# Kernel tuning notes

Hardware: AMD Instinct MI355X
Metric: run time of the kernel (lower is better)

The kernel has to match this reference:

```python
import jax, jax.numpy as jnp
import numpy as np

B, C, L = 8, 256, 4096
OC = C // 2  # out_channels default
EPS = 1e-5


def setup_inputs() -> dict:
    key = jax.random.key(0)
    ks = jax.random.split(key, 12)
    s_in = 1.0 / np.sqrt(C)   # conv1d default init scale (kaiming-uniform-ish)
    s_oc = 1.0 / np.sqrt(OC)
    return {
        "x": jax.random.normal(ks[0], (B, C, L), dtype=jnp.float32),
        "g_w": jax.random.uniform(ks[1], (OC, C), jnp.float32, -s_in, s_in),
        "g_b": jax.random.uniform(ks[2], (OC,), jnp.float32, -s_in, s_in),
        # theta/phi weights: nn.init.normal_(w, 0.02) -> mean 0.02, std 1
        "theta_w": 0.02 + jax.random.normal(ks[3], (OC, C), dtype=jnp.float32),
        "theta_b": jax.random.uniform(ks[4], (OC,), jnp.float32, -s_in, s_in),
        "phi_w": 0.02 + jax.random.normal(ks[5], (OC, C), dtype=jnp.float32),
        "phi_b": jax.random.uniform(ks[6], (OC,), jnp.float32, -s_in, s_in),
        "W_w": jax.random.uniform(ks[7], (C, OC), jnp.float32, -s_oc, s_oc),
        "W_b": jax.random.uniform(ks[8], (C,), jnp.float32, -s_oc, s_oc),
        # BN affine: init to zero in the original; use small random for a meaningful test
        "gamma": 0.1 * jax.random.normal(ks[9], (C,), dtype=jnp.float32),
        "beta": 0.1 * jax.random.normal(ks[10], (C,), dtype=jnp.float32),
    }


def reference(x, g_w, g_b, theta_w, theta_b, phi_w, phi_b, W_w, W_b, gamma, beta):
    # x: (b, c, l). 1x1 conv == per-position linear map over channels.
    g_x = jnp.einsum('oc,bcl->bol', g_w, x) + g_b[None, :, None]        # (b, oc, l)
    theta_x = jnp.einsum('oc,bcl->bol', theta_w, x) + theta_b[None, :, None]
    phi_x = jnp.einsum('oc,bcl->bol', phi_w, x) + phi_b[None, :, None]
    # f = theta^T phi : (b, l, l) quadratic score matrix (no softmax)
    f = jnp.einsum('bok,bom->bkm', theta_x, phi_x)
    N = f.shape[-1]
    # y = (f @ g^T) / N, returned in (b, oc, l) layout
    y = jnp.einsum('bkm,bom->bok', f, g_x) / N
    W_y = jnp.einsum('co,bol->bcl', W_w, y) + W_b[None, :, None]        # (b, c, l)
    # BatchNorm1d (training mode: batch statistics over (b, l), biased var)
    mean = jnp.mean(W_y, axis=(0, 2), keepdims=True)
    var = jnp.mean((W_y - mean) ** 2, axis=(0, 2), keepdims=True)
    W_y = (W_y - mean) * jax.lax.rsqrt(var + EPS)
    W_y = gamma[None, :, None] * W_y + beta[None, :, None]
    return W_y + x  # residual
```

## Files before the change

### kernel.cpp

```cpp
#include <hip/hip_runtime.h>
#include <hip/hip_bf16.h>

#define B_ 8
#define C_ 256
#define OC_ 128
#define L_ 4096
#define EPS_ 1e-5f
#define SPLITK 8

typedef unsigned short u16;
typedef __attribute__((ext_vector_type(4))) unsigned short u16x4;
typedef __attribute__((ext_vector_type(8))) unsigned short u16x8;
typedef __attribute__((ext_vector_type(4))) float f32x4;
typedef __attribute__((ext_vector_type(8))) short bf16x8;

__device__ inline u16 f2bf(float f) {
  union { __hip_bfloat16 h; u16 u; } v;
  v.h = __float2bfloat16(f);
  return v.u;
}
__device__ inline float bf2f(u16 u) {
  union { float f; unsigned u; } v;
  v.u = ((unsigned)u) << 16;
  return v.f;
}

__device__ inline void gload_lds16(const void* g, void* lds) {
  __builtin_amdgcn_global_load_lds(
      (const __attribute__((address_space(1))) unsigned int*)g,
      (__attribute__((address_space(3))) unsigned int*)lds, 16, 0, 0);
}

__device__ inline float blockReduceSum(float v, float* red, int nthreads) {
  int tid = threadIdx.x;
  red[tid] = v;
  __syncthreads();
  for (int s = nthreads >> 1; s > 0; s >>= 1) {
    if (tid < s) red[tid] += red[tid + s];
    __syncthreads();
  }
  float r = red[0];
  __syncthreads();
  return r;
}

__global__ __launch_bounds__(256) void k_cvt(const float* __restrict__ x,
                                             u16* __restrict__ Xb,
                                             u16* __restrict__ XbT) {
  __shared__ u16 T[64][72];
  const int b = blockIdx.z, c0 = blockIdx.y * 64, l0 = blockIdx.x * 64;
  const int tid = threadIdx.x;
#pragma unroll
  for (int it = 0; it < 4; ++it) {
    int idx = it * 256 + tid;
    int row = idx >> 4;
    int col = (idx & 15) << 2;
    size_t gi = ((size_t)(b * C_ + c0 + row)) * L_ + l0 + col;
    float4 v = *(const float4*)(x + gi);
    u16 u0 = f2bf(v.x), u1 = f2bf(v.y), u2 = f2bf(v.z), u3 = f2bf(v.w);
    u16x4 u = {u0, u1, u2, u3};
    *(u16x4*)(Xb + gi) = u;
    T[row][col] = u0; T[row][col + 1] = u1; T[row][col + 2] = u2; T[row][col + 3] = u3;
  }
  __syncthreads();
#pragma unroll
  for (int it = 0; it < 4; ++it) {
    int idx = it * 256 + tid;
    int lrow = idx >> 4;
    int ccol = (idx & 15) << 2;
    u16x4 u = {T[ccol][lrow], T[ccol + 1][lrow], T[ccol + 2][lrow], T[ccol + 3][lrow]};
    *(u16x4*)(XbT + ((size_t)b * L_ + l0 + lrow) * C_ + c0 + ccol) = u;
  }
}

__global__ __launch_bounds__(256) void k_rowsum(const u16* __restrict__ Xb,
                                                float* __restrict__ s) {
  int row = blockIdx.x;
  const u16x8* xr = (const u16x8*)(Xb + (size_t)row * L_);
  float acc = 0.f;
  for (int i = threadIdx.x; i < L_ / 8; i += 256) {
    u16x8 v = xr[i];
#pragma unroll
    for (int j = 0; j < 8; j++) acc += bf2f(v[j]);
  }
  __shared__ float red[256];
  float tot = blockReduceSum(acc, red, 256);
  if (threadIdx.x == 0) s[row] = tot;
}

__global__ __launch_bounds__(256) void k_xxt(const u16* __restrict__ Xb,
                                             float* __restrict__ Spart) {
  const int b = blockIdx.z, split = blockIdx.y;
  const int ti = blockIdx.x >> 1, tj = blockIdx.x & 1;
  __shared__ u16 lds[2 * 128 * 64];
  const int tid = threadIdx.x, lane = tid & 63;
  const int wid = tid >> 6, wr = wid >> 1, wc = wid & 1;
  const u16* Arows = Xb + ((size_t)b * C_ + ti * 128) * L_;
  const u16* Brows = Xb + ((size_t)b * C_ + tj * 128) * L_;
  const int k0 = split * (L_ / SPLITK);
  f32x4 acc[4][4] = {};
  for (int kt = 0; kt < L_ / SPLITK; kt += 64) {
    __syncthreads();
#pragma unroll
    for (int ch = 0; ch < 4; ch++) {
      int d = ch * 4096 + tid * 16;
      int row = d >> 7;
      int kb = (d & 127) ^ ((row & 7) << 4);
      gload_lds16(Arows + (size_t)row * L_ + k0 + kt + (kb >> 1), (char*)lds + d);
      gload_lds16(Brows + (size_t)row * L_ + k0 + kt + (kb >> 1), (char*)lds + 16384 + d);
    }
    asm volatile("s_waitcnt vmcnt(0)" ::: "memory");
    __syncthreads();
#pragma unroll
    for (int ks = 0; ks < 2; ks++) {
      bf16x8 af[4], bfr[4];
#pragma unroll
      for (int m = 0; m < 4; m++) {
        int row = wr * 64 + m * 16 + (lane & 15);
        int kb = ((ks << 6) + ((lane >> 4) << 4)) ^ ((row & 7) << 4);
        af[m] = *(const bf16x8*)((const char*)lds + row * 128 + kb);
      }
#pragma unroll
      for (int n = 0; n < 4; n++) {
        int row = wc * 64 + n * 16 + (lane & 15);
        int kb = ((ks << 6) + ((lane >> 4) << 4)) ^ ((row & 7) << 4);
        bfr[n] = *(const bf16x8*)((const char*)lds + 16384 + row * 128 + kb);
      }
#pragma unroll
      for (int m = 0; m < 4; m++)
#pragma unroll
        for (int n = 0; n < 4; n++)
          acc[m][n] = __builtin_amdgcn_mfma_f32_16x16x32_bf16(af[m], bfr[n], acc[m][n], 0, 0, 0);
    }
  }
  float* Sp = Spart + ((size_t)split * B_ + b) * C_ * C_;
#pragma unroll
  for (int m = 0; m < 4; m++)
#pragma unroll
    for (int n = 0; n < 4; n++) {
      int r0 = ti * 128 + wr * 64 + m * 16 + ((lane >> 4) << 2);
      int c0 = tj * 128 + wc * 64 + n * 16 + (lane & 15);
#pragma unroll
      for (int r = 0; r < 4; r++)
        Sp[(size_t)(r0 + r) * C_ + c0] = acc[m][n][r];
    }
}

__global__ __launch_bounds__(256) void k_sreduce(const float* __restrict__ Spart,
                                                 float* __restrict__ S) {
  size_t idx = (size_t)blockIdx.x * 256 + threadIdx.x;
  float acc = 0.f;
  for (int sp = 0; sp < SPLITK; sp++) acc += Spart[(size_t)sp * B_ * C_ * C_ + idx];
  S[idx] = acc;
}

__global__ __launch_bounds__(256) void k_mid1(const float* __restrict__ S,
                                              const float* __restrict__ s,
                                              const float* __restrict__ phi_w,
                                              const float* __restrict__ phi_b,
                                              const float* __restrict__ g_w,
                                              const float* __restrict__ g_b,
                                              float* __restrict__ M) {
  const int b = blockIdx.x >> 7, op = blockIdx.x & 127;
  const int tid = threadIdx.x;
  __shared__ float sl[C_], pw[C_], t2[C_], red[256];
  sl[tid] = s[b * C_ + tid];
  pw[tid] = phi_w[op * C_ + tid];
  __syncthreads();
  float ps_op = blockReduceSum(pw[tid] * sl[tid], red, 256);
  float phb = phi_b[op];
  const float* Sb = S + (size_t)b * C_ * C_;
  float t1 = 0.f;
  for (int cp = 0; cp < C_; cp++) t1 += pw[cp] * Sb[(size_t)cp * C_ + tid];
  t2[tid] = t1 + phb * sl[tid];
  __syncthreads();
  if (tid < OC_) {
    int o = tid;
    const float* gr = g_w + o * C_;
    float acc = 0.f;
    for (int c = 0; c < C_; c++) acc += t2[c] * gr[c];
    M[((size_t)b * OC_ + op) * OC_ + o] = acc + (ps_op + (float)L_ * phb) * g_b[o];
  }
}

__global__ __launch_bounds__(128) void k_mid2(const float* __restrict__ M,
                                              const float* __restrict__ W_w,
                                              const float* __restrict__ theta_w,
                                              const float* __restrict__ theta_b,
                                              const float* __restrict__ W_b,
                                              float* __restrict__ Q,
                                              float* __restrict__ q) {
  const int b = blockIdx.x >> 8, c = blockIdx.x & 255;
  const int tid = threadIdx.x;
  __shared__ float wr_[OC_], U_s[OC_], red[OC_];
  wr_[tid] = W_w[c * OC_ + tid];
  __syncthreads();
  const float* Mb = M + (size_t)b * OC_ * OC_;
  float acc = 0.f;
  for (int o = 0; o < OC_; o++) acc += wr_[o] * Mb[(size_t)tid * OC_ + o];
  acc *= (1.0f / (float)L_);
  U_s[tid] = acc;
  float tot = blockReduceSum(acc * theta_b[tid], red, OC_);
  if (tid == 0) q[b * C_ + c] = tot + W_b[c];
#pragma unroll
  for (int h = 0; h < 2; h++) {
    int ch = tid + h * OC_;
    float a2 = 0.f;
    for (int op = 0; op < OC_; op++) a2 += U_s[op] * theta_w[(size_t)op * C_ + ch];
    Q[((size_t)b * C_ + c) * C_ + ch] = a2;
  }
}

__global__ __launch_bounds__(256) void k_stats(const float* __restrict__ Q,
                                               const float* __restrict__ S,
                                               const float* __restrict__ s,
                                               const float* __restrict__ q,
                                               float* __restrict__ sum1,
                                               float* __restrict__ sum2) {
  int b = blockIdx.x >> 8, c = blockIdx.x & 255;
  __shared__ float qrow[C_];
  qrow[threadIdx.x] = Q[((size_t)b * C_ + c) * C_ + threadIdx.x];
  __syncthreads();
  const float* Sb = S + (size_t)b * C_ * C_;
  float r = 0.f;
  for (int cp = 0; cp < C_; cp++) r += qrow[cp] * Sb[(size_t)cp * C_ + threadIdx.x];
  __shared__ float red[C_];
  float e2 = blockReduceSum(r * qrow[threadIdx.x], red, C_);
  float qs = blockReduceSum(qrow[threadIdx.x] * s[b * C_ + threadIdx.x], red, C_);
  if (threadIdx.x == 0) {
    float qv = q[b * C_ + c];
    sum1[b * C_ + c] = qs + (float)L_ * qv;
    sum2[b * C_ + c] = e2 + 2.f * qv * qs + (float)L_ * qv * qv;
  }
}

__global__ __launch_bounds__(256) void k_build(const float* __restrict__ Q,
                                               const float* __restrict__ q,
                                               const float* __restrict__ sum1,
                                               const float* __restrict__ sum2,
                                               const float* __restrict__ gamma,
                                               const float* __restrict__ beta,
                                               u16* __restrict__ Qsb,
                                               float* __restrict__ qp) {
  int b = blockIdx.x >> 8, c = blockIdx.x & 255;
  float m = 0.f, e = 0.f;
  for (int bb = 0; bb < B_; bb++) {
    m += sum1[bb * C_ + c];
    e += sum2[bb * C_ + c];
  }
  const float inv_n = 1.f / (float)(B_ * L_);
  m *= inv_n;
  e *= inv_n;
  float var = e - m * m;
  float gsc = gamma[c] * rsqrtf(var + EPS_);
  size_t base = ((size_t)b * C_ + c) * C_;
  Qsb[base + threadIdx.x] = f2bf(gsc * Q[base + threadIdx.x]);
  if (threadIdx.x == 0) qp[b * C_ + c] = gsc * (q[b * C_ + c] - m) + beta[c];
}

__global__ __launch_bounds__(256) void k_out(const u16* __restrict__ Qsb,
                                             const float* __restrict__ qp,
                                             const u16* __restrict__ XbT,
                                             const u16* __restrict__ Xb,
                                             float* __restrict__ out) {
  const int b = blockIdx.z, ct = blockIdx.y, lt = blockIdx.x;
  __shared__ u16 lds[2 * 128 * 64];
  const int tid = threadIdx.x, lane = tid & 63;
  const int wid = tid >> 6, wr = wid >> 1, wc = wid & 1;
  const u16* Abase = Qsb + ((size_t)b * C_ + ct * 128) * C_;
  const u16* Bbase = XbT + ((size_t)b * L_ + lt * 128) * C_;
  f32x4 acc[4][4] = {};
  for (int k0 = 0; k0 < C_; k0 += 64) {
    __syncthreads();
#pragma unroll
    for (int ch = 0; ch < 4; ch++) {
      int d = ch * 4096 + tid * 16;
      int row = d >> 7;
      int kb = (d & 127) ^ ((row & 7) << 4);
      gload_lds16(Abase + (size_t)row * C_ + k0 + (kb >> 1), (char*)lds + d);
      gload_lds16(Bbase + (size_t)row * C_ + k0 + (kb >> 1), (char*)lds + 16384 + d);
    }
    asm volatile("s_waitcnt vmcnt(0)" ::: "memory");
    __syncthreads();
#pragma unroll
    for (int ks = 0; ks < 2; ks++) {
      bf16x8 af[4], bfr[4];
#pragma unroll
      for (int m = 0; m < 4; m++) {
        int row = wr * 64 + m * 16 + (lane & 15);
        int kb = ((ks << 6) + ((lane >> 4) << 4)) ^ ((row & 7) << 4);
        af[m] = *(const bf16x8*)((const char*)lds + row * 128 + kb);
      }
#pragma unroll
      for (int n = 0; n < 4; n++) {
        int row = wc * 64 + n * 16 + (lane & 15);
        int kb = ((ks << 6) + ((lane >> 4) << 4)) ^ ((row & 7) << 4);
        bfr[n] = *(const bf16x8*)((const char*)lds + 16384 + row * 128 + kb);
      }
#pragma unroll
      for (int m = 0; m < 4; m++)
#pragma unroll
        for (int n = 0; n < 4; n++)
          acc[m][n] = __builtin_amdgcn_mfma_f32_16x16x32_bf16(af[m], bfr[n], acc[m][n], 0, 0, 0);
    }
  }
#pragma unroll
  for (int m = 0; m < 4; m++)
#pragma unroll
    for (int n = 0; n < 4; n++) {
      int c = ct * 128 + wr * 64 + m * 16 + ((lane >> 4) << 2);
      int l = lt * 128 + wc * 64 + n * 16 + (lane & 15);
#pragma unroll
      for (int r = 0; r < 4; r++) {
        size_t gi = ((size_t)b * C_ + c + r) * L_ + l;
        out[gi] = acc[m][n][r] + bf2f(Xb[gi]) + qp[b * C_ + c + r];
      }
    }
}

extern "C" void kernel_launch(void* const* d_in, const int* in_sizes, int n_in,
                              void* d_out, int out_size, void* d_ws, size_t ws_size,
                              hipStream_t stream) {
  const float* x       = (const float*)d_in[0];
  const float* g_w     = (const float*)d_in[1];
  const float* g_b     = (const float*)d_in[2];
  const float* theta_w = (const float*)d_in[3];
  const float* theta_b = (const float*)d_in[4];
  const float* phi_w   = (const float*)d_in[5];
  const float* phi_b   = (const float*)d_in[6];
  const float* W_w     = (const float*)d_in[7];
  const float* W_b     = (const float*)d_in[8];
  const float* gamma   = (const float*)d_in[9];
  const float* beta    = (const float*)d_in[10];
  float* out = (float*)d_out;

  float* ws = (float*)d_ws;
  size_t off = 0;
  float* Spart = ws + off; off += (size_t)SPLITK * B_ * C_ * C_;
  float* S     = ws + off; off += (size_t)B_ * C_ * C_;
  float* s_    = ws + off; off += B_ * C_;
  float* M     = ws + off; off += (size_t)B_ * OC_ * OC_;
  float* qv    = ws + off; off += B_ * C_;
  float* Q     = ws + off; off += (size_t)B_ * C_ * C_;
  float* sum1  = ws + off; off += B_ * C_;
  float* sum2  = ws + off; off += B_ * C_;
  float* qp    = ws + off; off += B_ * C_;
  u16* Qsb = (u16*)(ws + off); off += (size_t)B_ * C_ * C_ / 2;
  u16* Xb  = (u16*)(ws + off); off += (size_t)B_ * C_ * L_ / 2;
  u16* XbT = (u16*)(ws + off); off += (size_t)B_ * C_ * L_ / 2;

  k_cvt<<<dim3(L_ / 64, C_ / 64, B_), 256, 0, stream>>>(x, Xb, XbT);
  k_rowsum<<<B_ * C_, 256, 0, stream>>>(Xb, s_);
  k_xxt<<<dim3(4, SPLITK, B_), 256, 0, stream>>>(Xb, Spart);
  k_sreduce<<<(B_ * C_ * C_) / 256, 256, 0, stream>>>(Spart, S);
  k_mid1<<<B_ * OC_, 256, 0, stream>>>(S, s_, phi_w, phi_b, g_w, g_b, M);
  k_mid2<<<B_ * C_, 128, 0, stream>>>(M, W_w, theta_w, theta_b, W_b, Q, qv);
  k_stats<<<B_ * C_, 256, 0, stream>>>(Q, S, s_, qv, sum1, sum2);
  k_build<<<B_ * C_, 256, 0, stream>>>(Q, qv, sum1, sum2, gamma, beta, Qsb, qp);
  k_out<<<dim3(L_ / 128, C_ / 128, B_), 256, 0, stream>>>(Qsb, qp, XbT, Xb, out);
}
```

Measured before the change: 143.1 us.

## Fuse rowsum, stats and build kernels into neighbours; cut launch count

The row sums of x are computed as per-tile partials inside the conversion kernel and finished in the split-K reduce kernel, which also transposes g_w. The stats and build kernels are folded into mid2 and the output GEMM: BN scale and shift are computed per tile, and Q is scaled and converted to bf16 on the fly from global memory rather than staged in LDS. mid1 and mid2 use transposed layouts for coalesced reads. This removes three launches and the Qsb round trip, but every output tile now re-reads fp32 Q from global and converts it per MFMA fragment, and the row sums now come from fp32 values instead of bf16.

```diff
diff --git a/kernel.cpp b/kernel.cpp
--- a/kernel.cpp
+++ b/kernel.cpp
@@ -10,7 +10,6 @@
 
 typedef unsigned short u16;
 typedef __attribute__((ext_vector_type(4))) unsigned short u16x4;
-typedef __attribute__((ext_vector_type(8))) unsigned short u16x8;
 typedef __attribute__((ext_vector_type(4))) float f32x4;
 typedef __attribute__((ext_vector_type(8))) short bf16x8;
 
@@ -46,8 +45,10 @@
 
 __global__ __launch_bounds__(256) void k_cvt(const float* __restrict__ x,
                                              u16* __restrict__ Xb,
-                                             u16* __restrict__ XbT) {
-  __shared__ u16 T[64][72];
+                                             u16* __restrict__ XbT,
+                                             float* __restrict__ spartial) {
+  __shared__ u16 T[64][73];
+  __shared__ float P[64][17];
   const int b = blockIdx.z, c0 = blockIdx.y * 64, l0 = blockIdx.x * 64;
   const int tid = threadIdx.x;
 #pragma unroll
@@ -61,8 +62,15 @@
     u16x4 u = {u0, u1, u2, u3};
     *(u16x4*)(Xb + gi) = u;
     T[row][col] = u0; T[row][col + 1] = u1; T[row][col + 2] = u2; T[row][col + 3] = u3;
-  }
-  __syncthreads();
+    P[row][idx & 15] = v.x + v.y + v.z + v.w;
+  }
+  __syncthreads();
+  if (tid < 64) {
+    float acc = 0.f;
+#pragma unroll
+    for (int j = 0; j < 16; j++) acc += P[tid][j];
+    spartial[(size_t)(b * C_ + c0 + tid) * 64 + blockIdx.x] = acc;
+  }
 #pragma unroll
   for (int it = 0; it < 4; ++it) {
     int idx = it * 256 + tid;
@@ -71,21 +79,6 @@
     u16x4 u = {T[ccol][lrow], T[ccol + 1][lrow], T[ccol + 2][lrow], T[ccol + 3][lrow]};
     *(u16x4*)(XbT + ((size_t)b * L_ + l0 + lrow) * C_ + c0 + ccol) = u;
   }
-}
-
-__global__ __launch_bounds__(256) void k_rowsum(const u16* __restrict__ Xb,
-                                                float* __restrict__ s) {
-  int row = blockIdx.x;
-  const u16x8* xr = (const u16x8*)(Xb + (size_t)row * L_);
-  float acc = 0.f;
-  for (int i = threadIdx.x; i < L_ / 8; i += 256) {
-    u16x8 v = xr[i];
-#pragma unroll
-    for (int j = 0; j < 8; j++) acc += bf2f(v[j]);
-  }
-  __shared__ float red[256];
-  float tot = blockReduceSum(acc, red, 256);
-  if (threadIdx.x == 0) s[row] = tot;
 }
 
 __global__ __launch_bounds__(256) void k_xxt(const u16* __restrict__ Xb,
@@ -147,20 +140,43 @@
 }
 
 __global__ __launch_bounds__(256) void k_sreduce(const float* __restrict__ Spart,
-                                                 float* __restrict__ S) {
-  size_t idx = (size_t)blockIdx.x * 256 + threadIdx.x;
-  float acc = 0.f;
-  for (int sp = 0; sp < SPLITK; sp++) acc += Spart[(size_t)sp * B_ * C_ * C_ + idx];
-  S[idx] = acc;
+                                                 const float* __restrict__ spartial,
+                                                 const float* __restrict__ g_w,
+                                                 float* __restrict__ S,
+                                                 float* __restrict__ s,
+                                                 float* __restrict__ gwT) {
+  const int bid = blockIdx.x, tid = threadIdx.x;
+  if (bid < (B_ * C_ * C_) / 256) {
+    size_t idx = (size_t)bid * 256 + tid;
+    float acc = 0.f;
+    for (int sp = 0; sp < SPLITK; sp++) acc += Spart[(size_t)sp * B_ * C_ * C_ + idx];
+    S[idx] = acc;
+  } else if (bid < (B_ * C_ * C_) / 256 + (B_ * C_) / 256) {
+    int idx2 = (bid - (B_ * C_ * C_) / 256) * 256 + tid;
+    const float4* sp = (const float4*)(spartial + (size_t)idx2 * 64);
+    float acc = 0.f;
+#pragma unroll
+    for (int i = 0; i < 16; i++) { float4 v = sp[i]; acc += v.x + v.y + v.z + v.w; }
+    s[idx2] = acc;
+  } else {
+    int t = bid - ((B_ * C_ * C_) / 256 + (B_ * C_) / 256);
+    int o = t * 8 + (tid & 7);
+    int cbase = (tid >> 3) * 8;
+#pragma unroll
+    for (int k = 0; k < 8; k++) {
+      int c = cbase + k;
+      gwT[c * OC_ + o] = g_w[o * C_ + c];
+    }
+  }
 }
 
 __global__ __launch_bounds__(256) void k_mid1(const float* __restrict__ S,
                                               const float* __restrict__ s,
                                               const float* __restrict__ phi_w,
                                               const float* __restrict__ phi_b,
-                                              const float* __restrict__ g_w,
+                                              const float* __restrict__ gwT,
                                               const float* __restrict__ g_b,
-                                              float* __restrict__ M) {
+                                              float* __restrict__ MT) {
   const int b = blockIdx.x >> 7, op = blockIdx.x & 127;
   const int tid = threadIdx.x;
   __shared__ float sl[C_], pw[C_], t2[C_], red[256];
@@ -174,101 +190,105 @@
   for (int cp = 0; cp < C_; cp++) t1 += pw[cp] * Sb[(size_t)cp * C_ + tid];
   t2[tid] = t1 + phb * sl[tid];
   __syncthreads();
+  const int o = tid & 127, half = tid >> 7;
+  float part = 0.f;
+  for (int cc = 0; cc < 128; cc++) {
+    int cidx = half * 128 + cc;
+    part += t2[cidx] * gwT[cidx * OC_ + o];
+  }
+  red[tid] = part;
+  __syncthreads();
   if (tid < OC_) {
-    int o = tid;
-    const float* gr = g_w + o * C_;
-    float acc = 0.f;
-    for (int c = 0; c < C_; c++) acc += t2[c] * gr[c];
-    M[((size_t)b * OC_ + op) * OC_ + o] = acc + (ps_op + (float)L_ * phb) * g_b[o];
-  }
-}
-
-__global__ __launch_bounds__(128) void k_mid2(const float* __restrict__ M,
-                                              const float* __restrict__ W_w,
-                                              const float* __restrict__ theta_w,
-                                              const float* __restrict__ theta_b,
-                                              const float* __restrict__ W_b,
-                                              float* __restrict__ Q,
-                                              float* __restrict__ q) {
+    float val = red[tid] + red[tid + 128] + (ps_op + (float)L_ * phb) * g_b[tid];
+    MT[((size_t)b * OC_ + tid) * OC_ + op] = val;
+  }
+}
+
+__global__ __launch_bounds__(128) void k_mid2stats(const float* __restrict__ MT,
+                                                   const float* __restrict__ W_w,
+                                                   const float* __restrict__ theta_w,
+                                                   const float* __restrict__ theta_b,
+                                                   const float* __restrict__ W_b,
+                                                   const float* __restrict__ S,
+                                                   const float* __restrict__ s,
+                                                   float* __restrict__ Q,
+                                                   float* __restrict__ qv,
+                                                   float* __restrict__ sum1,
+                                                   float* __restrict__ sum2) {
   const int b = blockIdx.x >> 8, c = blockIdx.x & 255;
   const int tid = threadIdx.x;
-  __shared__ float wr_[OC_], U_s[OC_], red[OC_];
+  __shared__ float wr_[OC_], U_s[OC_], red[OC_], qrow[C_];
   wr_[tid] = W_w[c * OC_ + tid];
   __syncthreads();
-  const float* Mb = M + (size_t)b * OC_ * OC_;
+  const float* MTb = MT + (size_t)b * OC_ * OC_;
   float acc = 0.f;
-  for (int o = 0; o < OC_; o++) acc += wr_[o] * Mb[(size_t)tid * OC_ + o];
+  for (int o = 0; o < OC_; o++) acc += wr_[o] * MTb[(size_t)o * OC_ + tid];
   acc *= (1.0f / (float)L_);
   U_s[tid] = acc;
   float tot = blockReduceSum(acc * theta_b[tid], red, OC_);
-  if (tid == 0) q[b * C_ + c] = tot + W_b[c];
+  float q_val = tot + W_b[c];
+  if (tid == 0) qv[b * C_ + c] = q_val;
+  float a2[2];
 #pragma unroll
   for (int h = 0; h < 2; h++) {
     int ch = tid + h * OC_;
-    float a2 = 0.f;
-    for (int op = 0; op < OC_; op++) a2 += U_s[op] * theta_w[(size_t)op * C_ + ch];
-    Q[((size_t)b * C_ + c) * C_ + ch] = a2;
-  }
-}
-
-__global__ __launch_bounds__(256) void k_stats(const float* __restrict__ Q,
-                                               const float* __restrict__ S,
-                                               const float* __restrict__ s,
-                                               const float* __restrict__ q,
-                                               float* __restrict__ sum1,
-                                               float* __restrict__ sum2) {
-  int b = blockIdx.x >> 8, c = blockIdx.x & 255;
-  __shared__ float qrow[C_];
-  qrow[threadIdx.x] = Q[((size_t)b * C_ + c) * C_ + threadIdx.x];
+    float a = 0.f;
+    for (int op = 0; op < OC_; op++) a += U_s[op] * theta_w[(size_t)op * C_ + ch];
+    a2[h] = a;
+    qrow[ch] = a;
+    Q[((size_t)b * C_ + c) * C_ + ch] = a;
+  }
   __syncthreads();
   const float* Sb = S + (size_t)b * C_ * C_;
-  float r = 0.f;
-  for (int cp = 0; cp < C_; cp++) r += qrow[cp] * Sb[(size_t)cp * C_ + threadIdx.x];
-  __shared__ float red[C_];
-  float e2 = blockReduceSum(r * qrow[threadIdx.x], red, C_);
-  float qs = blockReduceSum(qrow[threadIdx.x] * s[b * C_ + threadIdx.x], red, C_);
-  if (threadIdx.x == 0) {
-    float qv = q[b * C_ + c];
-    sum1[b * C_ + c] = qs + (float)L_ * qv;
-    sum2[b * C_ + c] = e2 + 2.f * qv * qs + (float)L_ * qv * qv;
-  }
-}
-
-__global__ __launch_bounds__(256) void k_build(const float* __restrict__ Q,
-                                               const float* __restrict__ q,
-                                               const float* __restrict__ sum1,
-                                               const float* __restrict__ sum2,
-                                               const float* __restrict__ gamma,
-                                               const float* __restrict__ beta,
-                                               u16* __restrict__ Qsb,
-                                               float* __restrict__ qp) {
-  int b = blockIdx.x >> 8, c = blockIdx.x & 255;
-  float m = 0.f, e = 0.f;
-  for (int bb = 0; bb < B_; bb++) {
-    m += sum1[bb * C_ + c];
-    e += sum2[bb * C_ + c];
-  }
-  const float inv_n = 1.f / (float)(B_ * L_);
-  m *= inv_n;
-  e *= inv_n;
-  float var = e - m * m;
-  float gsc = gamma[c] * rsqrtf(var + EPS_);
-  size_t base = ((size_t)b * C_ + c) * C_;
-  Qsb[base + threadIdx.x] = f2bf(gsc * Q[base + threadIdx.x]);
-  if (threadIdx.x == 0) qp[b * C_ + c] = gsc * (q[b * C_ + c] - m) + beta[c];
-}
-
-__global__ __launch_bounds__(256) void k_out(const u16* __restrict__ Qsb,
-                                             const float* __restrict__ qp,
+  float rq = 0.f, qssum = 0.f;
+#pragma unroll
+  for (int h = 0; h < 2; h++) {
+    int ch = tid + h * OC_;
+    float r = 0.f;
+    for (int cp = 0; cp < C_; cp++) r += qrow[cp] * Sb[(size_t)cp * C_ + ch];
+    rq += r * a2[h];
+    qssum += a2[h] * s[b * C_ + ch];
+  }
+  float e2 = blockReduceSum(rq, red, OC_);
+  float qs = blockReduceSum(qssum, red, OC_);
+  if (tid == 0) {
+    sum1[b * C_ + c] = qs + (float)L_ * q_val;
+    sum2[b * C_ + c] = e2 + 2.f * q_val * qs + (float)L_ * q_val * q_val;
+  }
+}
+
+__global__ __launch_bounds__(256) void k_out(const float* __restrict__ Q,
+                                             const float* __restrict__ qv,
+                                             const float* __restrict__ sum1,
+                                             const float* __restrict__ sum2,
+                                             const float* __restrict__ gamma,
+                                             const float* __restrict__ beta,
                                              const u16* __restrict__ XbT,
                                              const u16* __restrict__ Xb,
                                              float* __restrict__ out) {
   const int b = blockIdx.z, ct = blockIdx.y, lt = blockIdx.x;
-  __shared__ u16 lds[2 * 128 * 64];
+  __shared__ u16 lds[128 * 64];
+  __shared__ float gsc_s[128], qp_s[128];
   const int tid = threadIdx.x, lane = tid & 63;
   const int wid = tid >> 6, wr = wid >> 1, wc = wid & 1;
-  const u16* Abase = Qsb + ((size_t)b * C_ + ct * 128) * C_;
+  if (tid < 128) {
+    int c = ct * 128 + tid;
+    float m = 0.f, e = 0.f;
+#pragma unroll
+    for (int bb = 0; bb < B_; bb++) {
+      m += sum1[bb * C_ + c];
+      e += sum2[bb * C_ + c];
+    }
+    const float inv_n = 1.f / (float)(B_ * L_);
+    m *= inv_n;
+    e *= inv_n;
+    float var = e - m * m;
+    float g = gamma[c] * rsqrtf(var + EPS_);
+    gsc_s[tid] = g;
+    qp_s[tid] = g * (qv[b * C_ + c] - m) + beta[c];
+  }
   const u16* Bbase = XbT + ((size_t)b * L_ + lt * 128) * C_;
+  const float* Abase = Q + ((size_t)b * C_ + ct * 128) * C_;
   f32x4 acc[4][4] = {};
   for (int k0 = 0; k0 < C_; k0 += 64) {
     __syncthreads();
@@ -277,8 +297,7 @@
       int d = ch * 4096 + tid * 16;
       int row = d >> 7;
       int kb = (d & 127) ^ ((row & 7) << 4);
-      gload_lds16(Abase + (size_t)row * C_ + k0 + (kb >> 1), (char*)lds + d);
-      gload_lds16(Bbase + (size_t)row * C_ + k0 + (kb >> 1), (char*)lds + 16384 + d);
+      gload_lds16(Bbase + (size_t)row * C_ + k0 + (kb >> 1), (char*)lds + d);
     }
     asm volatile("s_waitcnt vmcnt(0)" ::: "memory");
     __syncthreads();
@@ -288,14 +307,23 @@
 #pragma unroll
       for (int m = 0; m < 4; m++) {
         int row = wr * 64 + m * 16 + (lane & 15);
-        int kb = ((ks << 6) + ((lane >> 4) << 4)) ^ ((row & 7) << 4);
-        af[m] = *(const bf16x8*)((const char*)lds + row * 128 + kb);
+        int kk = k0 + ks * 32 + ((lane >> 4) << 3);
+        float g = gsc_s[row];
+        const float* src = Abase + (size_t)row * C_ + kk;
+        float4 v0 = *(const float4*)src;
+        float4 v1 = *(const float4*)(src + 4);
+        bf16x8 a;
+        a[0] = (short)f2bf(g * v0.x); a[1] = (short)f2bf(g * v0.y);
+        a[2] = (short)f2bf(g * v0.z); a[3] = (short)f2bf(g * v0.w);
+        a[4] = (short)f2bf(g * v1.x); a[5] = (short)f2bf(g * v1.y);
+        a[6] = (short)f2bf(g * v1.z); a[7] = (short)f2bf(g * v1.w);
+        af[m] = a;
       }
 #pragma unroll
       for (int n = 0; n < 4; n++) {
         int row = wc * 64 + n * 16 + (lane & 15);
         int kb = ((ks << 6) + ((lane >> 4) << 4)) ^ ((row & 7) << 4);
-        bfr[n] = *(const bf16x8*)((const char*)lds + 16384 + row * 128 + kb);
+        bfr[n] = *(const bf16x8*)((const char*)lds + row * 128 + kb);
       }
 #pragma unroll
       for (int m = 0; m < 4; m++)
@@ -308,12 +336,13 @@
   for (int m = 0; m < 4; m++)
 #pragma unroll
     for (int n = 0; n < 4; n++) {
-      int c = ct * 128 + wr * 64 + m * 16 + ((lane >> 4) << 2);
+      int cl = wr * 64 + m * 16 + ((lane >> 4) << 2);
+      int c = ct * 128 + cl;
       int l = lt * 128 + wc * 64 + n * 16 + (lane & 15);
 #pragma unroll
       for (int r = 0; r < 4; r++) {
         size_t gi = ((size_t)b * C_ + c + r) * L_ + l;
-        out[gi] = acc[m][n][r] + bf2f(Xb[gi]) + qp[b * C_ + c + r];
+        out[gi] = acc[m][n][r] + bf2f(Xb[gi]) + qp_s[cl + r];
       }
     }
 }
@@ -336,26 +365,26 @@
 
   float* ws = (float*)d_ws;
   size_t off = 0;
-  float* Spart = ws + off; off += (size_t)SPLITK * B_ * C_ * C_;
-  float* S     = ws + off; off += (size_t)B_ * C_ * C_;
-  float* s_    = ws + off; off += B_ * C_;
-  float* M     = ws + off; off += (size_t)B_ * OC_ * OC_;
-  float* qv    = ws + off; off += B_ * C_;
-  float* Q     = ws + off; off += (size_t)B_ * C_ * C_;
-  float* sum1  = ws + off; off += B_ * C_;
-  float* sum2  = ws + off; off += B_ * C_;
-  float* qp    = ws + off; off += B_ * C_;
-  u16* Qsb = (u16*)(ws + off); off += (size_t)B_ * C_ * C_ / 2;
+  float* Spart    = ws + off; off += (size_t)SPLITK * B_ * C_ * C_;
+  float* S        = ws + off; off += (size_t)B_ * C_ * C_;
+  float* spartial = ws + off; off += (size_t)B_ * C_ * 64;
+  float* s_       = ws + off; off += B_ * C_;
+  float* gwT      = ws + off; off += C_ * OC_;
+  float* MT       = ws + off; off += (size_t)B_ * OC_ * OC_;
+  float* qv       = ws + off; off += B_ * C_;
+  float* Q        = ws + off; off += (size_t)B_ * C_ * C_;
+  float* sum1     = ws + off; off += B_ * C_;
+  float* sum2     = ws + off; off += B_ * C_;
   u16* Xb  = (u16*)(ws + off); off += (size_t)B_ * C_ * L_ / 2;
   u16* XbT = (u16*)(ws + off); off += (size_t)B_ * C_ * L_ / 2;
 
-  k_cvt<<<dim3(L_ / 64, C_ / 64, B_), 256, 0, stream>>>(x, Xb, XbT);
-  k_rowsum<<<B_ * C_, 256, 0, stream>>>(Xb, s_);
+  k_cvt<<<dim3(L_ / 64, C_ / 64, B_), 256, 0, stream>>>(x, Xb, XbT, spartial);
   k_xxt<<<dim3(4, SPLITK, B_), 256, 0, stream>>>(Xb, Spart);
-  k_sreduce<<<(B_ * C_ * C_) / 256, 256, 0, stream>>>(Spart, S);
-  k_mid1<<<B_ * OC_, 256, 0, stream>>>(S, s_, phi_w, phi_b, g_w, g_b, M);
-  k_mid2<<<B_ * C_, 128, 0, stream>>>(M, W_w, theta_w, theta_b, W_b, Q, qv);
-  k_stats<<<B_ * C_, 256, 0, stream>>>(Q, S, s_, qv, sum1, sum2);
-  k_build<<<B_ * C_, 256, 0, stream>>>(Q, qv, sum1, sum2, gamma, beta, Qsb, qp);
-  k_out<<<dim3(L_ / 128, C_ / 128, B_), 256, 0, stream>>>(Qsb, qp, XbT, Xb, out);
-}
+  k_sreduce<<<(B_ * C_ * C_) / 256 + (B_ * C_) / 256 + 16, 256, 0, stream>>>(
+      Spart, spartial, g_w, S, s_, gwT);
+  k_mid1<<<B_ * OC_, 256, 0, stream>>>(S, s_, phi_w, phi_b, gwT, g_b, MT);
+  k_mid2stats<<<B_ * C_, 128, 0, stream>>>(MT, W_w, theta_w, theta_b, W_b, S, s_,
+                                           Q, qv, sum1, sum2);
+  k_out<<<dim3(L_ / 128, C_ / 128, B_), 256, 0, stream>>>(Q, qv, sum1, sum2, gamma,
+                                                          beta, XbT, Xb, out);
+}
```

New measurement: 118.4 us. 1.21x faster.
